# Optimization experiments

Hardware: AMD Instinct MI355X
Metric: run time of the kernel (lower is better)

The kernel has to match this reference:

```python
import jax, jax.numpy as jnp
import numpy as np

N_DATA = 1200000
FEAT = 128
BATCH = 512
N_NEG = 4096
TEMP = 0.07
MOMENTUM = 0.5


def _l2norm(x):
    return x / jnp.maximum(jnp.linalg.norm(x, axis=-1, keepdims=True), 1e-12)


def setup_inputs() -> dict:
    key = jax.random.key(0)
    k1, k2, k3, k4, k5 = jax.random.split(key, 5)
    negatives = _l2norm(jax.random.normal(k1, (N_DATA, FEAT), dtype=jnp.float32))
    return {
        "student_feat": jax.random.normal(k2, (BATCH, FEAT), dtype=jnp.float32),
        "teacher_feat": jax.random.normal(k3, (BATCH, FEAT), dtype=jnp.float32),
        "negatives": negatives,
        "indices": jax.random.randint(k4, (BATCH,), 0, N_DATA, dtype=jnp.int64)
            if jax.config.read("jax_enable_x64") else jax.random.randint(k4, (BATCH,), 0, N_DATA, dtype=jnp.int32),
        "neg_indices": jax.random.randint(k5, (BATCH, N_NEG), 0, N_DATA, dtype=jnp.int32),
    }


def reference(student_feat, teacher_feat, negatives, indices, neg_indices):
    s = _l2norm(student_feat)                       # [B, D]
    t = _l2norm(teacher_feat)                       # [B, D]
    pos_sim = jnp.sum(s * t, axis=1) / TEMP         # [B]
    neg_feat = negatives[neg_indices]               # [B, K, D] gather from bank
    neg_sim = jnp.einsum('bd,bkd->bk', s, neg_feat) / TEMP  # [B, K]
    logits = jnp.concatenate([pos_sim[:, None], neg_sim], axis=1)  # [B, 1+K]
    # cross-entropy with label 0 for every row
    loss = jnp.mean(jax.nn.logsumexp(logits, axis=1) - logits[:, 0])
    # EMA scatter update + renormalize of touched rows (no-grad side effect)
    upd = MOMENTUM * negatives[indices] + (1.0 - MOMENTUM) * t
    upd = _l2norm(upd)
    new_negatives = negatives.at[indices].set(upd)
    return loss, new_negatives
```

## Files before the change

### kernel.cpp

```cpp
#include <hip/hip_runtime.h>

constexpr int   FEAT   = 128;
constexpr int   BATCH  = 512;
constexpr int   NNEG   = 4096;
constexpr long  NDATA  = 1200000;
constexpr int   CHUNKS = 8;
constexpr float INV_TEMP = 14.285714285714286f;
constexpr float LOG2E    = 1.4426950408889634f;
constexpr float LN2      = 0.6931471805599453f;
constexpr float K1       = INV_TEMP * LOG2E;

typedef float f4 __attribute__((ext_vector_type(4)));

__global__ __launch_bounds__(128) void prep_kernel(
    const float* __restrict__ sf, const float* __restrict__ tf,
    float* __restrict__ s_n, float* __restrict__ t_n, float* __restrict__ pos) {
  const int b = blockIdx.x, t = threadIdx.x;
  const float sv = sf[b * FEAT + t];
  const float tv = tf[b * FEAT + t];
  float ss = sv * sv, tt = tv * tv, st = sv * tv;
#pragma unroll
  for (int m = 1; m < 64; m <<= 1) {
    ss += __shfl_xor(ss, m);
    tt += __shfl_xor(tt, m);
    st += __shfl_xor(st, m);
  }
  __shared__ float sh[6];
  if ((t & 63) == 0) {
    const int w = t >> 6;
    sh[w * 3 + 0] = ss; sh[w * 3 + 1] = tt; sh[w * 3 + 2] = st;
  }
  __syncthreads();
  ss = sh[0] + sh[3]; tt = sh[1] + sh[4]; st = sh[2] + sh[5];
  const float snorm = fmaxf(sqrtf(ss), 1e-12f);
  const float tnorm = fmaxf(sqrtf(tt), 1e-12f);
  s_n[b * FEAT + t] = sv / snorm;
  t_n[b * FEAT + t] = tv / tnorm;
  if (t == 0) pos[b] = st / (snorm * tnorm) * INV_TEMP;
}

__global__ __launch_bounds__(256) void negsim_kernel(
    const float* __restrict__ neg, const int* __restrict__ nidx,
    const float* __restrict__ s_n, float* __restrict__ sumexp) {
  const int blk   = blockIdx.x;
  const int b     = blk >> 3;
  const int chunk = blk & (CHUNKS - 1);
  const int lane  = threadIdx.x & 63;
  const int w     = threadIdx.x >> 6;
  const float2 s2 = *(const float2*)(s_n + b * FEAT + 2 * lane);
  constexpr int KPC = NNEG / CHUNKS;
  constexpr int KPW = KPC / 4;
  const int* row_idx = nidx + b * NNEG + chunk * KPC + w * KPW;
  float acc = 0.f;
  for (int k = 0; k < KPW; k += 8) {
    int   idx[8];
    float p[8];
#pragma unroll
    for (int u = 0; u < 8; ++u) idx[u] = row_idx[k + u];
    float2 nv[8];
#pragma unroll
    for (int u = 0; u < 8; ++u)
      nv[u] = *(const float2*)(neg + (long)idx[u] * FEAT + 2 * lane);
#pragma unroll
    for (int u = 0; u < 8; ++u) p[u] = fmaf(s2.x, nv[u].x, s2.y * nv[u].y);
#pragma unroll
    for (int m = 1; m < 64; m <<= 1) {
#pragma unroll
      for (int u = 0; u < 8; ++u) p[u] += __shfl_xor(p[u], m);
    }
#pragma unroll
    for (int u = 0; u < 8; ++u) acc += exp2f(fmaf(p[u], K1, -K1));
  }
  __shared__ float part[4];
  if (lane == 0) part[w] = acc;
  __syncthreads();
  if (threadIdx.x == 0)
    sumexp[b * CHUNKS + chunk] = part[0] + part[1] + part[2] + part[3];
}

__global__ __launch_bounds__(512) void loss_kernel(
    const float* __restrict__ pos, const float* __restrict__ sumexp,
    float* __restrict__ out) {
  const int t = threadIdx.x;
  const float p = pos[t];
  float tot = exp2f(fmaf(p, LOG2E, -K1));
#pragma unroll
  for (int c = 0; c < CHUNKS; ++c) tot += sumexp[t * CHUNKS + c];
  float l = INV_TEMP + log2f(tot) * LN2 - p;
#pragma unroll
  for (int m = 1; m < 64; m <<= 1) l += __shfl_xor(l, m);
  __shared__ float sh[8];
  if ((t & 63) == 0) sh[t >> 6] = l;
  __syncthreads();
  if (t == 0) {
    float s = 0.f;
#pragma unroll
    for (int i = 0; i < 8; ++i) s += sh[i];
    out[0] = s / (float)BATCH;
  }
}

__global__ __launch_bounds__(256) void copy_kernel(
    const float* __restrict__ src, float* __restrict__ dst, long n4) {
  long i = (long)blockIdx.x * blockDim.x + threadIdx.x;
  const long stride = (long)gridDim.x * blockDim.x;
  for (; i < n4; i += stride) {
    const f4 v = __builtin_nontemporal_load((const f4*)src + i);
    float* d = dst + 4 * i;
    __builtin_nontemporal_store(v.x, d + 0);
    __builtin_nontemporal_store(v.y, d + 1);
    __builtin_nontemporal_store(v.z, d + 2);
    __builtin_nontemporal_store(v.w, d + 3);
  }
}

__global__ __launch_bounds__(128) void update_kernel(
    const float* __restrict__ neg, const float* __restrict__ t_n,
    const int* __restrict__ indices, float* __restrict__ dst) {
  const int b = blockIdx.x, t = threadIdx.x;
  __shared__ int sidx[BATCH];
  __shared__ int flag;
  if (t == 0) flag = 0;
  for (int j = t; j < BATCH; j += 128) sidx[j] = indices[j];
  __syncthreads();
  const int idx = sidx[b];
  int later = 0;
  for (int j = t; j < BATCH; j += 128)
    if (j > b && sidx[j] == idx) later = 1;
  if (later) flag = 1;
  __syncthreads();
  if (flag) return;
  const float u = 0.5f * neg[(long)idx * FEAT + t] + 0.5f * t_n[b * FEAT + t];
  float uu = u * u;
#pragma unroll
  for (int m = 1; m < 64; m <<= 1) uu += __shfl_xor(uu, m);
  __shared__ float sh2[2];
  if ((t & 63) == 0) sh2[t >> 6] = uu;
  __syncthreads();
  const float nrm = fmaxf(sqrtf(sh2[0] + sh2[1]), 1e-12f);
  dst[(long)idx * FEAT + t] = u / nrm;
}

extern "C" void kernel_launch(void* const* d_in, const int* in_sizes, int n_in,
                              void* d_out, int out_size, void* d_ws, size_t ws_size,
                              hipStream_t stream) {
  const float* student   = (const float*)d_in[0];
  const float* teacher   = (const float*)d_in[1];
  const float* negatives = (const float*)d_in[2];
  const int*   indices   = (const int*)d_in[3];
  const int*   neg_idx   = (const int*)d_in[4];
  float* out = (float*)d_out;

  float* ws     = (float*)d_ws;
  float* s_n    = ws;
  float* t_n    = s_n + BATCH * FEAT;
  float* pos    = t_n + BATCH * FEAT;
  float* sumexp = pos + BATCH;

  prep_kernel<<<BATCH, 128, 0, stream>>>(student, teacher, s_n, t_n, pos);
  negsim_kernel<<<BATCH * CHUNKS, 256, 0, stream>>>(negatives, neg_idx, s_n, sumexp);
  loss_kernel<<<1, 512, 0, stream>>>(pos, sumexp, out);
  copy_kernel<<<2048, 256, 0, stream>>>(negatives, out + 1, NDATA * (long)FEAT / 4);
  update_kernel<<<BATCH, 128, 0, stream>>>(negatives, t_n, indices, out + 1);
}
```

Measured before the change: 402.1 us.

## Run bank copy concurrently with negative-similarity blocks and merge loss with update

```diff
diff --git a/kernel.cpp b/kernel.cpp
--- a/kernel.cpp
+++ b/kernel.cpp
@@ -5,6 +5,7 @@
 constexpr int   NNEG   = 4096;
 constexpr long  NDATA  = 1200000;
 constexpr int   CHUNKS = 8;
+constexpr int   NCOPY  = 1024;
 constexpr float INV_TEMP = 14.285714285714286f;
 constexpr float LOG2E    = 1.4426950408889634f;
 constexpr float LN2      = 0.6931471805599453f;
@@ -39,10 +40,26 @@
   if (t == 0) pos[b] = st / (snorm * tnorm) * INV_TEMP;
 }
 
-__global__ __launch_bounds__(256) void negsim_kernel(
+__global__ __launch_bounds__(256) void work_kernel(
     const float* __restrict__ neg, const int* __restrict__ nidx,
-    const float* __restrict__ s_n, float* __restrict__ sumexp) {
-  const int blk   = blockIdx.x;
+    const float* __restrict__ s_n, float* __restrict__ sumexp,
+    float* __restrict__ dst) {
+  __shared__ float part[4];
+  if (blockIdx.x < NCOPY) {
+    const long n4 = NDATA * (long)FEAT / 4;
+    long i = (long)blockIdx.x * blockDim.x + threadIdx.x;
+    const long stride = (long)NCOPY * blockDim.x;
+    for (; i < n4; i += stride) {
+      const f4 v = *((const f4*)neg + i);
+      float* d = dst + 4 * i;
+      __builtin_nontemporal_store(v.x, d + 0);
+      __builtin_nontemporal_store(v.y, d + 1);
+      __builtin_nontemporal_store(v.z, d + 2);
+      __builtin_nontemporal_store(v.w, d + 3);
+    }
+    return;
+  }
+  const int blk   = blockIdx.x - NCOPY;
   const int b     = blk >> 3;
   const int chunk = blk & (CHUNKS - 1);
   const int lane  = threadIdx.x & 63;
@@ -71,74 +88,63 @@
 #pragma unroll
     for (int u = 0; u < 8; ++u) acc += exp2f(fmaf(p[u], K1, -K1));
   }
-  __shared__ float part[4];
   if (lane == 0) part[w] = acc;
   __syncthreads();
   if (threadIdx.x == 0)
     sumexp[b * CHUNKS + chunk] = part[0] + part[1] + part[2] + part[3];
 }
 
-__global__ __launch_bounds__(512) void loss_kernel(
+__global__ __launch_bounds__(256) void finish_kernel(
     const float* __restrict__ pos, const float* __restrict__ sumexp,
-    float* __restrict__ out) {
+    const float* __restrict__ neg, const float* __restrict__ t_n,
+    const int* __restrict__ indices, float* __restrict__ out) {
   const int t = threadIdx.x;
-  const float p = pos[t];
-  float tot = exp2f(fmaf(p, LOG2E, -K1));
+  if (blockIdx.x == 0) {
+    float lsum = 0.f;
 #pragma unroll
-  for (int c = 0; c < CHUNKS; ++c) tot += sumexp[t * CHUNKS + c];
-  float l = INV_TEMP + log2f(tot) * LN2 - p;
+    for (int r = t; r < BATCH; r += 256) {
+      const float p = pos[r];
+      float tot = exp2f(fmaf(p, LOG2E, -K1));
 #pragma unroll
-  for (int m = 1; m < 64; m <<= 1) l += __shfl_xor(l, m);
-  __shared__ float sh[8];
-  if ((t & 63) == 0) sh[t >> 6] = l;
-  __syncthreads();
-  if (t == 0) {
-    float s = 0.f;
+      for (int c = 0; c < CHUNKS; ++c) tot += sumexp[r * CHUNKS + c];
+      lsum += INV_TEMP + log2f(tot) * LN2 - p;
+    }
 #pragma unroll
-    for (int i = 0; i < 8; ++i) s += sh[i];
-    out[0] = s / (float)BATCH;
+    for (int m = 1; m < 64; m <<= 1) lsum += __shfl_xor(lsum, m);
+    __shared__ float sh[4];
+    if ((t & 63) == 0) sh[t >> 6] = lsum;
+    __syncthreads();
+    if (t == 0) out[0] = (sh[0] + sh[1] + sh[2] + sh[3]) / (float)BATCH;
+    return;
   }
-}
-
-__global__ __launch_bounds__(256) void copy_kernel(
-    const float* __restrict__ src, float* __restrict__ dst, long n4) {
-  long i = (long)blockIdx.x * blockDim.x + threadIdx.x;
-  const long stride = (long)gridDim.x * blockDim.x;
-  for (; i < n4; i += stride) {
-    const f4 v = __builtin_nontemporal_load((const f4*)src + i);
-    float* d = dst + 4 * i;
-    __builtin_nontemporal_store(v.x, d + 0);
-    __builtin_nontemporal_store(v.y, d + 1);
-    __builtin_nontemporal_store(v.z, d + 2);
-    __builtin_nontemporal_store(v.w, d + 3);
-  }
-}
-
-__global__ __launch_bounds__(128) void update_kernel(
-    const float* __restrict__ neg, const float* __restrict__ t_n,
-    const int* __restrict__ indices, float* __restrict__ dst) {
-  const int b = blockIdx.x, t = threadIdx.x;
+  const int b = blockIdx.x - 1;
+  float* dst = out + 1;
   __shared__ int sidx[BATCH];
   __shared__ int flag;
   if (t == 0) flag = 0;
-  for (int j = t; j < BATCH; j += 128) sidx[j] = indices[j];
+  for (int j = t; j < BATCH; j += 256) sidx[j] = indices[j];
   __syncthreads();
   const int idx = sidx[b];
   int later = 0;
-  for (int j = t; j < BATCH; j += 128)
+  for (int j = t; j < BATCH; j += 256)
     if (j > b && sidx[j] == idx) later = 1;
   if (later) flag = 1;
   __syncthreads();
   if (flag) return;
-  const float u = 0.5f * neg[(long)idx * FEAT + t] + 0.5f * t_n[b * FEAT + t];
-  float uu = u * u;
+  float u = 0.f, uu = 0.f;
+  if (t < FEAT) {
+    u = 0.5f * neg[(long)idx * FEAT + t] + 0.5f * t_n[b * FEAT + t];
+    uu = u * u;
+  }
 #pragma unroll
   for (int m = 1; m < 64; m <<= 1) uu += __shfl_xor(uu, m);
   __shared__ float sh2[2];
-  if ((t & 63) == 0) sh2[t >> 6] = uu;
+  if (t == 0 || t == 64) sh2[t >> 6] = uu;
   __syncthreads();
-  const float nrm = fmaxf(sqrtf(sh2[0] + sh2[1]), 1e-12f);
-  dst[(long)idx * FEAT + t] = u / nrm;
+  if (t < FEAT) {
+    const float nrm = fmaxf(sqrtf(sh2[0] + sh2[1]), 1e-12f);
+    dst[(long)idx * FEAT + t] = u / nrm;
+  }
 }
 
 extern "C" void kernel_launch(void* const* d_in, const int* in_sizes, int n_in,
@@ -158,8 +164,8 @@
   float* sumexp = pos + BATCH;
 
   prep_kernel<<<BATCH, 128, 0, stream>>>(student, teacher, s_n, t_n, pos);
-  negsim_kernel<<<BATCH * CHUNKS, 256, 0, stream>>>(negatives, neg_idx, s_n, sumexp);
-  loss_kernel<<<1, 512, 0, stream>>>(pos, sumexp, out);
-  copy_kernel<<<2048, 256, 0, stream>>>(negatives, out + 1, NDATA * (long)FEAT / 4);
-  update_kernel<<<BATCH, 128, 0, stream>>>(negatives, t_n, indices, out + 1);
+  work_kernel<<<NCOPY + BATCH * CHUNKS, 256, 0, stream>>>(
+      negatives, neg_idx, s_n, sumexp, out + 1);
+  finish_kernel<<<1 + BATCH, 256, 0, stream>>>(
+      pos, sumexp, negatives, t_n, indices, out);
 }
```

Measured after the change: 397.5 us. No clear change (-1.1%).
